# Optimization experiments

Measured on AMD Instinct MI355X. Metric: run time of the kernel, lower is better.

Reference implementation:

```python
import jax, jax.numpy as jnp
import numpy as np

B, D_IN, D_HID, D_OUT = 16384, 256, 512, 256
E, K = 8, 2  # expert_num, activate_num


def setup_inputs() -> dict:
    key = jax.random.key(0)
    ks = jax.random.split(key, 6)
    s_in = 1.0 / np.sqrt(D_IN)
    s_hid = 1.0 / np.sqrt(D_HID)
    return {
        "x": jax.random.normal(ks[0], (B, D_IN), dtype=jnp.float32),
        "Wg": jax.random.normal(ks[1], (D_IN, E), dtype=jnp.float32) * s_in,
        "W1": jax.random.normal(ks[2], (E, D_IN, D_HID), dtype=jnp.float32) * s_in,
        "b1": jnp.zeros((E, D_HID), dtype=jnp.float32),
        "W2": jax.random.normal(ks[3], (E, D_HID, D_OUT), dtype=jnp.float32) * s_hid,
        "b2": jnp.zeros((E, D_OUT), dtype=jnp.float32),
    }


def reference(x, Wg, W1, b1, W2, b2):
    # Gating: logits -> top-k -> softmax over the k selected logits.
    # (nn.Dropout on gate logits is identity at inference.)
    gate_logits = x @ Wg                              # [B, E]
    weights, selected = jax.lax.top_k(gate_logits, K)  # [B, K], [B, K]
    weights = jax.nn.softmax(weights.astype(jnp.float32), axis=1).astype(x.dtype)

    # Expert compute, vectorized over experts (same math as the per-expert
    # gather/compute/scatter loop; tokens not routed to expert e get weight 0).
    h = jax.nn.relu(jnp.einsum("bd,edh->ebh", x, W1) + b1[:, None, :])  # [E, B, H]
    expert_out = jnp.einsum("ebh,eho->ebo", h, W2) + b2[:, None, :]      # [E, B, O]

    # Combine weights: combine[b, e] = sum_k weights[b,k] * [selected[b,k]==e]
    one_hot = jax.nn.one_hot(selected, E, dtype=x.dtype)  # [B, K, E]
    combine = jnp.einsum("bk,bke->be", weights, one_hot)  # [B, E]
    results = jnp.einsum("be,ebo->bo", combine, expert_out)  # [B, O]
    return results
```

## Files before the change

kernel.cpp:

```cpp
#include <hip/hip_runtime.h>
#include <hip/hip_bf16.h>

typedef __bf16 bf16x8 __attribute__((ext_vector_type(8)));
typedef __bf16 bf16x4 __attribute__((ext_vector_type(4)));
typedef float f32x4 __attribute__((ext_vector_type(4)));

#define NTOK 16384
#define DIN  256
#define DHID 512
#define DOUT 256
#define NEXP 8

#define MFMA16(a, b, c) __builtin_amdgcn_mfma_f32_16x16x32_bf16(a, b, c, 0, 0, 0)
#define GLD16(gp, lp)                                                       \
  __builtin_amdgcn_global_load_lds(                                         \
      (__attribute__((address_space(1))) void*)(gp),                        \
      (__attribute__((address_space(3))) void*)(lp), 16, 0, 0)

__global__ __launch_bounds__(256) void wcvt_kernel(const float* __restrict__ src,
                                                   __bf16* __restrict__ dst,
                                                   int K, int nsh) {
  int e = blockIdx.y;
  int flat = blockIdx.x * 256 + threadIdx.x;
  int N = 1 << nsh;
  int kg = flat >> nsh;
  int n = flat & (N - 1);
  const float* s = src + ((size_t)e * K + (size_t)kg * 8) * N + n;
  bf16x8 t;
#pragma unroll
  for (int j = 0; j < 8; ++j) t[j] = (__bf16)s[(size_t)j * N];
  *(bf16x8*)(dst + (size_t)((e << nsh) + n) * K + kg * 8) = t;
}

__global__ __launch_bounds__(256) void gate_kernel(const float* __restrict__ x,
                                                   const float* __restrict__ wg,
                                                   int* __restrict__ cnt,
                                                   int* __restrict__ btok,
                                                   float* __restrict__ bw,
                                                   __bf16* __restrict__ xbf) {
  __shared__ int lcnt[NEXP];
  __shared__ int lbase[NEXP];
  const int tid = threadIdx.x;
  if (tid < NEXP) lcnt[tid] = 0;

  const int sub = tid & 7;
  const int tslot = tid >> 3;
  const int token = blockIdx.x * 32 + tslot;
  const f32x4* xr = (const f32x4*)(x + (size_t)token * DIN + sub * 32);
  const float* wr0 = wg + (size_t)sub * 32 * NEXP;

  bf16x8 xb[4];
  f32x4 p0 = {0.f, 0.f, 0.f, 0.f}, p1 = {0.f, 0.f, 0.f, 0.f};
#pragma unroll
  for (int j4 = 0; j4 < 8; ++j4) {
    f32x4 xv = xr[j4];
    const float* wr = wr0 + j4 * 32;
#pragma unroll
    for (int d = 0; d < 4; ++d) {
      float xs_ = xv[d];
      p0 += xs_ * *(const f32x4*)(wr + 8 * d);
      p1 += xs_ * *(const f32x4*)(wr + 8 * d + 4);
      xb[j4 >> 1][(j4 & 1) * 4 + d] = (__bf16)xs_;
    }
  }
  {
    bf16x8* xdst = (bf16x8*)(xbf + (size_t)token * DIN + sub * 32);
#pragma unroll
    for (int i = 0; i < 4; ++i) xdst[i] = xb[i];
  }

  double acc[NEXP];
#pragma unroll
  for (int d = 0; d < 4; ++d) {
    acc[d] = (double)p0[d];
    acc[4 + d] = (double)p1[d];
  }
#pragma unroll
  for (int off = 1; off < 8; off <<= 1)
#pragma unroll
    for (int e = 0; e < NEXP; ++e) acc[e] += __shfl_xor(acc[e], off, 64);

  __syncthreads();

  int i1 = 0, i2 = 0, o1 = 0, o2 = 0;
  float w1 = 0.f, w2 = 0.f;
  if (sub == 0) {
    double bv1 = acc[0];
#pragma unroll
    for (int e = 1; e < NEXP; ++e)
      if (acc[e] > bv1) { bv1 = acc[e]; i1 = e; }
    double bv2 = -1e300;
#pragma unroll
    for (int e = 0; e < NEXP; ++e)
      if (e != i1 && acc[e] > bv2) { bv2 = acc[e]; i2 = e; }
    float dd = expf((float)(bv2 - bv1));
    w1 = 1.0f / (1.0f + dd);
    w2 = dd * w1;
    o1 = atomicAdd(&lcnt[i1], 1);
    o2 = atomicAdd(&lcnt[i2], 1);
  }
  __syncthreads();
  if (tid < NEXP) lbase[tid] = atomicAdd(&cnt[tid], lcnt[tid]);
  __syncthreads();
  if (sub == 0) {
    int s1 = lbase[i1] + o1, s2 = lbase[i2] + o2;
    btok[i1 * NTOK + s1] = token;
    bw[i1 * NTOK + s1] = w1;
    btok[i2 * NTOK + s2] = token;
    bw[i2 * NTOK + s2] = w2;
  }
}

__global__ __launch_bounds__(256, 2) void ffn_kernel(
    const __bf16* __restrict__ xbf, const __bf16* __restrict__ w1bf,
    const __bf16* __restrict__ w2bf, const float* __restrict__ b1g,
    const float* __restrict__ b2g, const int* __restrict__ cnt,
    const int* __restrict__ btok, const float* __restrict__ bw,
    float* __restrict__ out) {
  __shared__ __align__(16) __bf16 wb1[64 * 256];
  __shared__ __align__(16) __bf16 wb2[256 * 64];
  __shared__ __align__(16) __bf16 hs[64 * 64];
  __shared__ int tok[64];
  __shared__ float wgt[64];
  __shared__ float b2s[DOUT];

  const int tid = threadIdx.x;
  const int e = blockIdx.y;
  const int ce = cnt[e];
  const int start = blockIdx.x * 64;
  if (start >= ce) return;

  if (tid < 64) {
    int idx = start + tid;
    bool v = idx < ce;
    tok[tid] = v ? btok[e * NTOK + idx] : 0;
    wgt[tid] = v ? bw[e * NTOK + idx] : 0.0f;
  }
  b2s[tid] = b2g[e * DOUT + tid];
  __syncthreads();

  const int lane = tid & 63;
  const int wid = tid >> 6;
  const int l15 = lane & 15;
  const int quad = lane >> 4;
  const int wh = wid >> 1;
  const int wt = wid & 1;

  bf16x8 xA[2][8];
  {
    const __bf16* r0 = xbf + (size_t)tok[wt * 32 + l15] * DIN + quad * 8;
    const __bf16* r1 = xbf + (size_t)tok[wt * 32 + 16 + l15] * DIN + quad * 8;
#pragma unroll
    for (int kc = 0; kc < 8; ++kc) {
      xA[0][kc] = *(const bf16x8*)(r0 + kc * 32);
      xA[1][kc] = *(const bf16x8*)(r1 + kc * 32);
    }
  }

  f32x4 acc[2][8];
#pragma unroll
  for (int mi = 0; mi < 2; ++mi)
#pragma unroll
    for (int ni = 0; ni < 8; ++ni) acc[mi][ni] = (f32x4){0.f, 0.f, 0.f, 0.f};

  const __bf16* w1e = w1bf + (size_t)e * DHID * DIN;
  const __bf16* w2e = w2bf + (size_t)e * DOUT * DHID;
  const int r1n = lane >> 5, s1 = lane & 31;
  const int r2n = lane >> 3, s2 = lane & 7;

  for (int hc = 0; hc < 8; ++hc) {
    __syncthreads();

#pragma unroll
    for (int j = 0; j < 8; ++j) {
      int W = wid * 8 + j;
      int n = 2 * W + r1n;
      int c = s1 ^ (n & 31);
      GLD16(w1e + (size_t)(hc * 64 + n) * DIN + c * 8, wb1 + W * 512);
    }
#pragma unroll
    for (int j = 0; j < 8; ++j) {
      int W = wid * 8 + j;
      int n = 8 * W + r2n;
      int c = s2 ^ (n & 7);
      GLD16(w2e + (size_t)n * DHID + hc * 64 + c * 8, wb2 + W * 512);
    }
    __syncthreads();

    f32x4 S[2][2];
#pragma unroll
    for (int nh = 0; nh < 2; ++nh)
#pragma unroll
      for (int mt = 0; mt < 2; ++mt) S[nh][mt] = (f32x4){0.f, 0.f, 0.f, 0.f};
#pragma unroll
    for (int kc = 0; kc < 8; ++kc) {
      int sl = ((kc << 2) | quad) ^ l15;
      bf16x8 w0 = *(const bf16x8*)((const char*)wb1 + (wh * 32 + l15) * 512 + sl * 16);
      bf16x8 w1v = *(const bf16x8*)((const char*)wb1 + (wh * 32 + 16 + l15) * 512 + (sl ^ 16) * 16);
      S[0][0] = MFMA16(w0, xA[0][kc], S[0][0]);
      S[0][1] = MFMA16(w0, xA[1][kc], S[0][1]);
      S[1][0] = MFMA16(w1v, xA[0][kc], S[1][0]);
      S[1][1] = MFMA16(w1v, xA[1][kc], S[1][1]);
    }
#pragma unroll
    for (int nh = 0; nh < 2; ++nh) {
      int kl = wh * 32 + nh * 16 + quad * 4;
      f32x4 bv = *(const f32x4*)(b1g + e * DHID + hc * 64 + kl);
      int cpart = kl >> 3;
      int boff = (kl & 7) << 1;
#pragma unroll
      for (int mt = 0; mt < 2; ++mt) {
        int m = wt * 32 + mt * 16 + l15;
        bf16x4 pk;
#pragma unroll
        for (int r = 0; r < 4; ++r)
          pk[r] = (__bf16)fmaxf(S[nh][mt][r] + bv[r], 0.f);
        *(bf16x4*)((char*)hs + m * 128 + ((cpart ^ (m & 7)) << 4) + boff) = pk;
      }
    }
    __syncthreads();

#pragma unroll
    for (int kc = 0; kc < 2; ++kc) {
      int c = (kc << 2) | quad;
      int m0 = wh * 32 + l15, m1 = m0 + 16;
      bf16x8 h0 = *(const bf16x8*)((const char*)hs + m0 * 128 + ((c ^ (m0 & 7)) << 4));
      bf16x8 h1 = *(const bf16x8*)((const char*)hs + m1 * 128 + ((c ^ (m1 & 7)) << 4));
#pragma unroll
      for (int ni = 0; ni < 8; ++ni) {
        int n = wt * 128 + ni * 16 + l15;
        bf16x8 bb = *(const bf16x8*)((const char*)wb2 + n * 128 + ((c ^ (n & 7)) << 4));
        acc[0][ni] = MFMA16(h0, bb, acc[0][ni]);
        acc[1][ni] = MFMA16(h1, bb, acc[1][ni]);
      }
    }
  }

#pragma unroll
  for (int mi = 0; mi < 2; ++mi) {
#pragma unroll
    for (int r = 0; r < 4; ++r) {
      int m = wh * 32 + mi * 16 + quad * 4 + r;
      float wv = wgt[m];
      float* orow = out + (size_t)tok[m] * DOUT;
#pragma unroll
      for (int ni = 0; ni < 8; ++ni) {
        int n = wt * 128 + ni * 16 + l15;
        atomicAdd(orow + n, wv * (acc[mi][ni][r] + b2s[n]));
      }
    }
  }
}

extern "C" void kernel_launch(void* const* d_in, const int* in_sizes, int n_in,
                              void* d_out, int out_size, void* d_ws, size_t ws_size,
                              hipStream_t stream) {
  const float* x = (const float*)d_in[0];
  const float* Wg = (const float*)d_in[1];
  const float* W1 = (const float*)d_in[2];
  const float* b1 = (const float*)d_in[3];
  const float* W2 = (const float*)d_in[4];
  const float* b2 = (const float*)d_in[5];
  float* out = (float*)d_out;

  char* ws = (char*)d_ws;
  int* cnt = (int*)(ws + 0);
  int* btok = (int*)(ws + 256);
  float* bw = (float*)(ws + 524544);
  __bf16* xbf = (__bf16*)(ws + 1048832);
  __bf16* w1bf = (__bf16*)(ws + 9437440);
  __bf16* w2bf = (__bf16*)(ws + 11534592);

  hipMemsetAsync(out, 0, (size_t)NTOK * DOUT * sizeof(float), stream);
  hipMemsetAsync(cnt, 0, NEXP * sizeof(int), stream);

  wcvt_kernel<<<dim3(64, NEXP), dim3(256), 0, stream>>>(W1, w1bf, DIN, 9);
  wcvt_kernel<<<dim3(64, NEXP), dim3(256), 0, stream>>>(W2, w2bf, DHID, 8);
  gate_kernel<<<dim3(NTOK / 32), dim3(256), 0, stream>>>(x, Wg, cnt, btok, bw, xbf);
  ffn_kernel<<<dim3(256, NEXP), dim3(256), 0, stream>>>(xbf, w1bf, w2bf, b1, b2,
                                                        cnt, btok, bw, out);
}
```

Baseline: 184.2 us.

## Replace atomic scatter with bf16 per-slot partials, compact expert grid, 32x32 MFMA

The FFN kernel now writes each token's weighted expert output as bf16 into one of two partial buffers, picked by the routing slot encoded in the token index. A new combine kernel sums the two buffers into the fp32 output, which removes the output memset and the fp32 global atomics. The grid is compacted to a 1D launch that maps blocks to experts using prefix counts, so there are fewer idle blocks. MFMA moves from 16x16x32 to 32x32x16 tiles, and the two weight-conversion launches are merged into one. The cost is an extra pass over the partial buffers and rounding the partial outputs to bf16.

New measurement: 161.7 us. 1.14x faster.

```diff
diff --git a/kernel.cpp b/kernel.cpp
--- a/kernel.cpp
+++ b/kernel.cpp
@@ -4,6 +4,7 @@
 typedef __bf16 bf16x8 __attribute__((ext_vector_type(8)));
 typedef __bf16 bf16x4 __attribute__((ext_vector_type(4)));
 typedef float f32x4 __attribute__((ext_vector_type(4)));
+typedef float f32x16 __attribute__((ext_vector_type(16)));
 
 #define NTOK 16384
 #define DIN  256
@@ -11,17 +12,23 @@
 #define DOUT 256
 #define NEXP 8
 
-#define MFMA16(a, b, c) __builtin_amdgcn_mfma_f32_16x16x32_bf16(a, b, c, 0, 0, 0)
+#define MFMA32(a, b, c) __builtin_amdgcn_mfma_f32_32x32x16_bf16(a, b, c, 0, 0, 0)
 #define GLD16(gp, lp)                                                       \
   __builtin_amdgcn_global_load_lds(                                         \
       (__attribute__((address_space(1))) void*)(gp),                        \
       (__attribute__((address_space(3))) void*)(lp), 16, 0, 0)
 
-__global__ __launch_bounds__(256) void wcvt_kernel(const float* __restrict__ src,
-                                                   __bf16* __restrict__ dst,
-                                                   int K, int nsh) {
+__global__ __launch_bounds__(256) void wcvt_kernel(const float* __restrict__ w1,
+                                                   const float* __restrict__ w2,
+                                                   __bf16* __restrict__ w1bf,
+                                                   __bf16* __restrict__ w2bf) {
   int e = blockIdx.y;
-  int flat = blockIdx.x * 256 + threadIdx.x;
+  bool isW1 = blockIdx.x < 64;
+  int flat = (isW1 ? blockIdx.x : blockIdx.x - 64) * 256 + threadIdx.x;
+  const float* src = isW1 ? w1 : w2;
+  __bf16* dst = isW1 ? w1bf : w2bf;
+  int K = isW1 ? DIN : DHID;
+  int nsh = isW1 ? 9 : 8;
   int N = 1 << nsh;
   int kg = flat >> nsh;
   int n = flat & (N - 1);
@@ -106,7 +113,7 @@
     int s1 = lbase[i1] + o1, s2 = lbase[i2] + o2;
     btok[i1 * NTOK + s1] = token;
     bw[i1 * NTOK + s1] = w1;
-    btok[i2 * NTOK + s2] = token;
+    btok[i2 * NTOK + s2] = token | 16384;
     bw[i2 * NTOK + s2] = w2;
   }
 }
@@ -116,24 +123,37 @@
     const __bf16* __restrict__ w2bf, const float* __restrict__ b1g,
     const float* __restrict__ b2g, const int* __restrict__ cnt,
     const int* __restrict__ btok, const float* __restrict__ bw,
-    float* __restrict__ out) {
+    __bf16* __restrict__ pout) {
   __shared__ __align__(16) __bf16 wb1[64 * 256];
   __shared__ __align__(16) __bf16 wb2[256 * 64];
   __shared__ __align__(16) __bf16 hs[64 * 64];
   __shared__ int tok[64];
+  __shared__ int srow[64];
   __shared__ float wgt[64];
   __shared__ float b2s[DOUT];
 
+  int b = blockIdx.x;
+  int e = -1, start = 0;
+  {
+    int a0 = 0;
+#pragma unroll
+    for (int q = 0; q < NEXP; ++q) {
+      int t = (cnt[q] + 63) >> 6;
+      if (e < 0 && b < a0 + t) { e = q; start = (b - a0) * 64; }
+      a0 += t;
+    }
+  }
+  if (e < 0) return;
+  const int ce = cnt[e];
+
   const int tid = threadIdx.x;
-  const int e = blockIdx.y;
-  const int ce = cnt[e];
-  const int start = blockIdx.x * 64;
-  if (start >= ce) return;
-
   if (tid < 64) {
     int idx = start + tid;
     bool v = idx < ce;
-    tok[tid] = v ? btok[e * NTOK + idx] : 0;
+    int entry = v ? btok[e * NTOK + idx] : 0;
+    int t = entry & 16383;
+    tok[tid] = t;
+    srow[tid] = (entry >> 14) * NTOK + t;
     wgt[tid] = v ? bw[e * NTOK + idx] : 0.0f;
   }
   b2s[tid] = b2g[e * DOUT + tid];
@@ -141,32 +161,29 @@
 
   const int lane = tid & 63;
   const int wid = tid >> 6;
-  const int l15 = lane & 15;
-  const int quad = lane >> 4;
+  const int hi = lane >> 5;
+  const int l31 = lane & 31;
   const int wh = wid >> 1;
   const int wt = wid & 1;
-
-  bf16x8 xA[2][8];
+  const int wo = wid;
+
+  bf16x8 xB[16];
   {
-    const __bf16* r0 = xbf + (size_t)tok[wt * 32 + l15] * DIN + quad * 8;
-    const __bf16* r1 = xbf + (size_t)tok[wt * 32 + 16 + l15] * DIN + quad * 8;
-#pragma unroll
-    for (int kc = 0; kc < 8; ++kc) {
-      xA[0][kc] = *(const bf16x8*)(r0 + kc * 32);
-      xA[1][kc] = *(const bf16x8*)(r1 + kc * 32);
-    }
-  }
-
-  f32x4 acc[2][8];
-#pragma unroll
-  for (int mi = 0; mi < 2; ++mi)
-#pragma unroll
-    for (int ni = 0; ni < 8; ++ni) acc[mi][ni] = (f32x4){0.f, 0.f, 0.f, 0.f};
+    const __bf16* xr = xbf + (size_t)tok[wt * 32 + l31] * DIN + hi * 8;
+#pragma unroll
+    for (int kw = 0; kw < 16; ++kw) xB[kw] = *(const bf16x8*)(xr + kw * 16);
+  }
 
   const __bf16* w1e = w1bf + (size_t)e * DHID * DIN;
   const __bf16* w2e = w2bf + (size_t)e * DOUT * DHID;
-  const int r1n = lane >> 5, s1 = lane & 31;
-  const int r2n = lane >> 3, s2 = lane & 7;
+
+  f32x16 acc[2][2];
+#pragma unroll
+  for (int ai = 0; ai < 2; ++ai)
+#pragma unroll
+    for (int bi = 0; bi < 2; ++bi)
+#pragma unroll
+      for (int r = 0; r < 16; ++r) acc[ai][bi][r] = 0.f;
 
   for (int hc = 0; hc < 8; ++hc) {
     __syncthreads();
@@ -174,82 +191,101 @@
 #pragma unroll
     for (int j = 0; j < 8; ++j) {
       int W = wid * 8 + j;
-      int n = 2 * W + r1n;
-      int c = s1 ^ (n & 31);
-      GLD16(w1e + (size_t)(hc * 64 + n) * DIN + c * 8, wb1 + W * 512);
-    }
-#pragma unroll
-    for (int j = 0; j < 8; ++j) {
-      int W = wid * 8 + j;
-      int n = 8 * W + r2n;
-      int c = s2 ^ (n & 7);
-      GLD16(w2e + (size_t)n * DHID + hc * 64 + c * 8, wb2 + W * 512);
+      int n1 = 2 * W + hi;
+      int s1 = l31 ^ (n1 & 31);
+      GLD16(w1e + (size_t)(hc * 64 + n1) * DIN + s1 * 8, wb1 + W * 512);
+      int n2 = 8 * W + (lane >> 3);
+      int s2 = (lane & 7) ^ (n2 & 7);
+      GLD16(w2e + (size_t)n2 * DHID + hc * 64 + s2 * 8, wb2 + W * 512);
     }
     __syncthreads();
 
-    f32x4 S[2][2];
-#pragma unroll
-    for (int nh = 0; nh < 2; ++nh)
-#pragma unroll
-      for (int mt = 0; mt < 2; ++mt) S[nh][mt] = (f32x4){0.f, 0.f, 0.f, 0.f};
-#pragma unroll
-    for (int kc = 0; kc < 8; ++kc) {
-      int sl = ((kc << 2) | quad) ^ l15;
-      bf16x8 w0 = *(const bf16x8*)((const char*)wb1 + (wh * 32 + l15) * 512 + sl * 16);
-      bf16x8 w1v = *(const bf16x8*)((const char*)wb1 + (wh * 32 + 16 + l15) * 512 + (sl ^ 16) * 16);
-      S[0][0] = MFMA16(w0, xA[0][kc], S[0][0]);
-      S[0][1] = MFMA16(w0, xA[1][kc], S[0][1]);
-      S[1][0] = MFMA16(w1v, xA[0][kc], S[1][0]);
-      S[1][1] = MFMA16(w1v, xA[1][kc], S[1][1]);
-    }
-#pragma unroll
-    for (int nh = 0; nh < 2; ++nh) {
-      int kl = wh * 32 + nh * 16 + quad * 4;
-      f32x4 bv = *(const f32x4*)(b1g + e * DHID + hc * 64 + kl);
-      int cpart = kl >> 3;
-      int boff = (kl & 7) << 1;
-#pragma unroll
-      for (int mt = 0; mt < 2; ++mt) {
-        int m = wt * 32 + mt * 16 + l15;
-        bf16x4 pk;
-#pragma unroll
-        for (int r = 0; r < 4; ++r)
-          pk[r] = (__bf16)fmaxf(S[nh][mt][r] + bv[r], 0.f);
-        *(bf16x4*)((char*)hs + m * 128 + ((cpart ^ (m & 7)) << 4) + boff) = pk;
+    f32x16 S;
+#pragma unroll
+    for (int r = 0; r < 16; ++r) S[r] = 0.f;
+#pragma unroll
+    for (int kw = 0; kw < 16; ++kw) {
+      int row = wh * 32 + l31;
+      int s = (kw * 2 + hi) ^ (row & 31);
+      bf16x8 a = *(const bf16x8*)((const char*)wb1 + row * 512 + s * 16);
+      S = MFMA32(a, xB[kw], S);
+    }
+#pragma unroll
+    for (int g = 0; g < 4; ++g) {
+      int hl = wh * 32 + 8 * g + 4 * hi;
+      f32x4 bv = *(const f32x4*)(b1g + e * DHID + hc * 64 + hl);
+      bf16x4 pk;
+#pragma unroll
+      for (int r = 0; r < 4; ++r)
+        pk[r] = (__bf16)fmaxf(S[4 * g + r] + bv[r], 0.f);
+      int m = wt * 32 + l31;
+      int slot = (hl >> 3) ^ (m & 7);
+      *(bf16x4*)((char*)hs + m * 128 + slot * 16 + (hl & 7) * 2) = pk;
+    }
+    __syncthreads();
+
+#pragma unroll
+    for (int kw = 0; kw < 4; ++kw) {
+      bf16x8 wf[2], hf[2];
+#pragma unroll
+      for (int ai = 0; ai < 2; ++ai) {
+        int row = wo * 64 + ai * 32 + l31;
+        int s = (kw * 2 + hi) ^ (row & 7);
+        wf[ai] = *(const bf16x8*)((const char*)wb2 + row * 128 + s * 16);
       }
-    }
-    __syncthreads();
-
-#pragma unroll
-    for (int kc = 0; kc < 2; ++kc) {
-      int c = (kc << 2) | quad;
-      int m0 = wh * 32 + l15, m1 = m0 + 16;
-      bf16x8 h0 = *(const bf16x8*)((const char*)hs + m0 * 128 + ((c ^ (m0 & 7)) << 4));
-      bf16x8 h1 = *(const bf16x8*)((const char*)hs + m1 * 128 + ((c ^ (m1 & 7)) << 4));
-#pragma unroll
-      for (int ni = 0; ni < 8; ++ni) {
-        int n = wt * 128 + ni * 16 + l15;
-        bf16x8 bb = *(const bf16x8*)((const char*)wb2 + n * 128 + ((c ^ (n & 7)) << 4));
-        acc[0][ni] = MFMA16(h0, bb, acc[0][ni]);
-        acc[1][ni] = MFMA16(h1, bb, acc[1][ni]);
+#pragma unroll
+      for (int bi = 0; bi < 2; ++bi) {
+        int m = bi * 32 + l31;
+        int s = (kw * 2 + hi) ^ (m & 7);
+        hf[bi] = *(const bf16x8*)((const char*)hs + m * 128 + s * 16);
       }
-    }
-  }
-
-#pragma unroll
-  for (int mi = 0; mi < 2; ++mi) {
-#pragma unroll
-    for (int r = 0; r < 4; ++r) {
-      int m = wh * 32 + mi * 16 + quad * 4 + r;
-      float wv = wgt[m];
-      float* orow = out + (size_t)tok[m] * DOUT;
-#pragma unroll
-      for (int ni = 0; ni < 8; ++ni) {
-        int n = wt * 128 + ni * 16 + l15;
-        atomicAdd(orow + n, wv * (acc[mi][ni][r] + b2s[n]));
+      acc[0][0] = MFMA32(wf[0], hf[0], acc[0][0]);
+      acc[0][1] = MFMA32(wf[0], hf[1], acc[0][1]);
+      acc[1][0] = MFMA32(wf[1], hf[0], acc[1][0]);
+      acc[1][1] = MFMA32(wf[1], hf[1], acc[1][1]);
+    }
+  }
+
+#pragma unroll
+  for (int bi = 0; bi < 2; ++bi) {
+    int tm = bi * 32 + l31;
+    if (start + tm < ce) {
+      float wv = wgt[tm];
+      __bf16* prow = pout + (size_t)srow[tm] * DOUT;
+#pragma unroll
+      for (int ai = 0; ai < 2; ++ai) {
+#pragma unroll
+        for (int g = 0; g < 4; ++g) {
+          int o0 = wo * 64 + ai * 32 + 8 * g + 4 * hi;
+          f32x4 bv = *(const f32x4*)(&b2s[o0]);
+          bf16x4 pk;
+#pragma unroll
+          for (int r = 0; r < 4; ++r)
+            pk[r] = (__bf16)(wv * (acc[ai][bi][4 * g + r] + bv[r]));
+          *(bf16x4*)(prow + o0) = pk;
+        }
       }
     }
   }
+}
+
+__global__ __launch_bounds__(256) void combine_kernel(const __bf16* __restrict__ pout,
+                                                      float* __restrict__ out) {
+  int f = blockIdx.x * 256 + threadIdx.x;
+  bf16x8 a = *(const bf16x8*)(pout + (size_t)f * 8);
+  bf16x8 b = *(const bf16x8*)(pout + (size_t)NTOK * DOUT + (size_t)f * 8);
+  float4 o0, o1;
+  o0.x = (float)a[0] + (float)b[0];
+  o0.y = (float)a[1] + (float)b[1];
+  o0.z = (float)a[2] + (float)b[2];
+  o0.w = (float)a[3] + (float)b[3];
+  o1.x = (float)a[4] + (float)b[4];
+  o1.y = (float)a[5] + (float)b[5];
+  o1.z = (float)a[6] + (float)b[6];
+  o1.w = (float)a[7] + (float)b[7];
+  float4* dst = (float4*)(out + (size_t)f * 8);
+  dst[0] = o0;
+  dst[1] = o1;
 }
 
 extern "C" void kernel_launch(void* const* d_in, const int* in_sizes, int n_in,
@@ -270,13 +306,13 @@
   __bf16* xbf = (__bf16*)(ws + 1048832);
   __bf16* w1bf = (__bf16*)(ws + 9437440);
   __bf16* w2bf = (__bf16*)(ws + 11534592);
-
-  hipMemsetAsync(out, 0, (size_t)NTOK * DOUT * sizeof(float), stream);
+  __bf16* pout = (__bf16*)(ws + 13631744);
+
   hipMemsetAsync(cnt, 0, NEXP * sizeof(int), stream);
 
-  wcvt_kernel<<<dim3(64, NEXP), dim3(256), 0, stream>>>(W1, w1bf, DIN, 9);
-  wcvt_kernel<<<dim3(64, NEXP), dim3(256), 0, stream>>>(W2, w2bf, DHID, 8);
+  wcvt_kernel<<<dim3(128, NEXP), dim3(256), 0, stream>>>(W1, W2, w1bf, w2bf);
   gate_kernel<<<dim3(NTOK / 32), dim3(256), 0, stream>>>(x, Wg, cnt, btok, bw, xbf);
-  ffn_kernel<<<dim3(256, NEXP), dim3(256), 0, stream>>>(xbf, w1bf, w2bf, b1, b2,
-                                                        cnt, btok, bw, out);
-}
+  ffn_kernel<<<dim3(520), dim3(256), 0, stream>>>(xbf, w1bf, w2bf, b1, b2,
+                                                  cnt, btok, bw, pout);
+  combine_kernel<<<dim3(NTOK * DOUT / 8 / 256), dim3(256), 0, stream>>>(pout, out);
+}
```
